# Performance work log

Measured on AMD Instinct MI355X. Metric: run time of the kernel, lower is better.

## Reference

```python
import jax, jax.numpy as jnp
import numpy as np


def setup_inputs() -> dict:
    key = jax.random.key(0)
    k1, k2 = jax.random.split(key)
    x = jax.random.normal(k1, (3000, 800, 8), dtype=jnp.float32)
    y = jax.random.normal(k2, (3000, 800, 8), dtype=jnp.float32)
    return {"x": x, "y": y}


def _cumtrapz(a):
    # torch.cumulative_trapezoid along last axis (unit spacing): len nt-1
    return jnp.cumsum(0.5 * (a[:, 1:] + a[:, :-1]), axis=1)


def _wd1d(x, y):
    nt = x.shape[0]
    # flatten (ntraces, nchannels) -> batch of independent 1D traces [N, nt]
    syn = x.reshape(nt, -1).T
    obs = y.reshape(nt, -1).T
    # per trace-pair joint minimum (torch.min(torch.min(syn), torch.min(obs)))
    mind = jnp.minimum(syn.min(axis=1, keepdims=True), obs.min(axis=1, keepdims=True))
    syn = syn - mind
    obs = obs - mind
    cdf_syn = _cumtrapz(syn)                                  # [N, nt-1]
    cdf_obs = _cumtrapz(obs)                                  # [N, nt-1]
    syn_norm = cdf_syn / jnp.sum(cdf_syn, axis=1, keepdims=True)
    obs_norm = cdf_obs / jnp.sum(cdf_obs, axis=1, keepdims=True)
    # torch.searchsorted default (right=False) == jnp side='left'
    idx = jax.vmap(lambda a, v: jnp.searchsorted(a, v, side='left'))(obs_norm, syn_norm)
    idx = jnp.minimum(idx, nt - 1)                            # clamp; t[idx] == idx since t = arange(nt)
    t_tail = jnp.arange(1, nt, dtype=jnp.int32)               # t[1:]
    diff = (t_tail[None, :] - idx).astype(syn_norm.dtype)
    return jnp.sum(diff * diff * syn_norm)


def reference(x, y):
    return _wd1d(x, y)
```

## Files before the change

kernel.cpp:

```cpp
#include <hip/hip_runtime.h>

#define NT   3000
#define NK   2999
#define NTR  6400
#define NPAIR 3200
#define CCH  64
#define KCH  47
#define GRP  8

#define TRIW 4498500.0f
#define FINF 3.4e38f

__global__ __launch_bounds__(128) void kA(
    const float* __restrict__ X, const float* __restrict__ Y,
    float* __restrict__ offx, float* __restrict__ offy,
    float* __restrict__ cmn,
    float* __restrict__ wsxA, float* __restrict__ wsyA)
{
    const int p = blockIdx.x * 128 + threadIdx.x;
    const int n = 2 * p;
    const int c = blockIdx.y;
    const int j0 = c * KCH;
    const int j1 = min(NK, j0 + KCH);

    const float2* __restrict__ X2 = (const float2*)X;
    const float2* __restrict__ Y2 = (const float2*)Y;

    float2 xp = X2[j0 * NPAIR + p];
    float2 yp = Y2[j0 * NPAIR + p];
    float mn0 = fminf(xp.x, yp.x), mn1 = fminf(xp.y, yp.y);
    float sx0 = 0.f, sx1 = 0.f, sy0 = 0.f, sy1 = 0.f;
    float wx0 = 0.f, wx1 = 0.f, wy0 = 0.f, wy1 = 0.f;

    #pragma unroll 4
    for (int j = j0; j < j1; ++j) {
        const float2 xn = X2[(j + 1) * NPAIR + p];
        const float2 yn = Y2[(j + 1) * NPAIR + p];
        const float w = (float)(NK - j);
        float s;
        s = 0.5f * (xp.x + xn.x); sx0 += s; wx0 = fmaf(s, w, wx0);
        s = 0.5f * (xp.y + xn.y); sx1 += s; wx1 = fmaf(s, w, wx1);
        s = 0.5f * (yp.x + yn.x); sy0 += s; wy0 = fmaf(s, w, wy0);
        s = 0.5f * (yp.y + yn.y); sy1 += s; wy1 = fmaf(s, w, wy1);
        mn0 = fminf(mn0, fminf(xn.x, yn.x));
        mn1 = fminf(mn1, fminf(xn.y, yn.y));
        xp = xn; yp = yn;
    }

    const int o = c * NTR + n;
    *(float2*)&offx[o] = make_float2(sx0, sx1);
    *(float2*)&offy[o] = make_float2(sy0, sy1);
    *(float2*)&cmn[o]  = make_float2(mn0, mn1);
    atomicAdd(&wsxA[n], wx0); atomicAdd(&wsxA[n + 1], wx1);
    atomicAdd(&wsyA[n], wy0); atomicAdd(&wsyA[n + 1], wy1);
}

__global__ __launch_bounds__(256) void kB(
    float* __restrict__ offx, float* __restrict__ offy,
    const float* __restrict__ cmn,
    const float* __restrict__ wsxA, const float* __restrict__ wsyA,
    float* __restrict__ mindA, float* __restrict__ SsynA,
    float* __restrict__ SobsA, float* __restrict__ out)
{
    const int n = blockIdx.x * 256 + threadIdx.x;
    if (blockIdx.x == 0 && threadIdx.x == 0) out[0] = 0.0f;

    float mn = FINF;
    for (int c = 0; c < CCH; ++c) mn = fminf(mn, cmn[c * NTR + n]);

    float rx = 0.f, ry = 0.f;
    for (int c = 0; c < CCH; ++c) {
        const int o = c * NTR + n;
        const float tx = offx[o], ty = offy[o];
        offx[o] = rx; offy[o] = ry;
        rx += tx; ry += ty;
    }

    mindA[n] = mn;
    SsynA[n] = wsxA[n] - mn * TRIW;
    SobsA[n] = wsyA[n] - mn * TRIW;
}

__global__ __launch_bounds__(256) void kC(
    const float* __restrict__ X, const float* __restrict__ Y,
    const float* __restrict__ offx, const float* __restrict__ offy,
    const float* __restrict__ mindA, const float* __restrict__ SsynA,
    const float* __restrict__ SobsA, float* __restrict__ out)
{
    const int n = blockIdx.x * 256 + threadIdx.x;
    const int c = blockIdx.y;
    const int j0 = c * KCH;
    const int j1 = min(NK, j0 + KCH);

    const float mind = mindA[n];
    const float Ssyn = SsynA[n];
    const float Sobs = SobsA[n];
    const float invS = 1.0f / Ssyn;

    float cs = offx[c * NTR + n];
    float xp = X[j0 * NTR + n];
    float acc = 0.f;

    int   mbase;
    float co;
    float ylast;
    float o[GRP];
    float co8, y8;

    #define FILL() do {                                                   \
        float yl_ = ylast, cc_ = co;                                      \
        _Pragma("unroll")                                                 \
        for (int i = 0; i < GRP; ++i) {                                   \
            const int m_ = mbase + i;                                     \
            const int ml_ = (m_ < NK) ? (m_ + 1) : NK;                    \
            const float yn_ = Y[ml_ * NTR + n];                           \
            cc_ += 0.5f * (yl_ + yn_);                                    \
            yl_ = yn_;                                                    \
            const float v_ = (cc_ - (float)(m_ + 1) * mind) * Ssyn;       \
            o[i] = (m_ < NK) ? v_ : FINF;                                 \
        }                                                                 \
        co8 = cc_; y8 = yl_;                                              \
    } while (0)

    #define COUNT(tgt, cnt) do {                                          \
        cnt = 0;                                                          \
        _Pragma("unroll")                                                 \
        for (int i = 0; i < GRP; ++i) cnt += (o[i] < (tgt)) ? 1 : 0;      \
    } while (0)

    {
        const float xn = X[(j0 + 1) * NTR + n];
        cs += 0.5f * (xp + xn); xp = xn;
        const float synp = cs - (float)(j0 + 1) * mind;
        const float target = synp * Sobs;

        int cc = 0;
        for (int c2 = min(CCH - 1, c + 2); c2 >= 1; --c2) {
            const float v = (offy[c2 * NTR + n] - (float)(c2 * KCH) * mind) * Ssyn;
            if (v < target) { cc = c2; break; }
        }
        mbase = cc * KCH;
        co = offy[cc * NTR + n];
        ylast = Y[mbase * NTR + n];
        FILL();
        int cnt; COUNT(target, cnt);
        while (cnt == GRP) {
            mbase += GRP; co = co8; ylast = y8;
            FILL();
            COUNT(target, cnt);
        }
        const float diff = (float)(j0 + 1 - (mbase + cnt));
        acc = fmaf(diff * diff, synp * invS, acc);
    }

    for (int k = j0 + 1; k < j1; ++k) {
        const float xn = X[(k + 1) * NTR + n];
        cs += 0.5f * (xp + xn); xp = xn;
        const float synp = cs - (float)(k + 1) * mind;
        const float target = synp * Sobs;

        int cnt; COUNT(target, cnt);
        while (cnt == GRP) {
            mbase += GRP; co = co8; ylast = y8;
            FILL();
            COUNT(target, cnt);
        }
        const float diff = (float)(k + 1 - (mbase + cnt));
        acc = fmaf(diff * diff, synp * invS, acc);
    }

    #undef FILL
    #undef COUNT

    __shared__ float red[256];
    red[threadIdx.x] = acc;
    __syncthreads();
    for (int s = 128; s > 0; s >>= 1) {
        if (threadIdx.x < s) red[threadIdx.x] += red[threadIdx.x + s];
        __syncthreads();
    }
    if (threadIdx.x == 0) atomicAdd(out, red[0]);
}

extern "C" void kernel_launch(void* const* d_in, const int* in_sizes, int n_in,
                              void* d_out, int out_size, void* d_ws, size_t ws_size,
                              hipStream_t stream)
{
    const float* X = (const float*)d_in[0];
    const float* Y = (const float*)d_in[1];
    float* out = (float*)d_out;

    float* w = (float*)d_ws;
    float* offx  = w;
    float* offy  = offx + CCH * NTR;
    float* cmn   = offy + CCH * NTR;
    float* wsxA  = cmn  + CCH * NTR;
    float* wsyA  = wsxA + NTR;
    float* mindA = wsyA + NTR;
    float* SsynA = mindA + NTR;
    float* SobsA = SsynA + NTR;

    hipMemsetAsync(wsxA, 0, 2 * NTR * sizeof(float), stream);

    dim3 gA(NPAIR / 128, CCH), bA(128);
    dim3 gB(NTR / 256), bB(256);
    dim3 gC(NTR / 256, CCH), bC(256);

    kA<<<gA, bA, 0, stream>>>(X, Y, offx, offy, cmn, wsxA, wsyA);
    kB<<<gB, bB, 0, stream>>>(offx, offy, cmn, wsxA, wsyA,
                              mindA, SsynA, SobsA, out);
    kC<<<gC, bC, 0, stream>>>(X, Y, offx, offy, mindA, SsynA, SobsA, out);
}
```

Before: 317.8 us.

## Precompute per-chunk search start in kB and remap kC blocks for locality

```diff
diff --git a/kernel.cpp b/kernel.cpp
--- a/kernel.cpp
+++ b/kernel.cpp
@@ -7,6 +7,7 @@
 #define CCH  64
 #define KCH  47
 #define GRP  8
+#define GT   64
 
 #define TRIW 4498500.0f
 #define FINF 3.4e38f
@@ -32,7 +33,7 @@
     float sx0 = 0.f, sx1 = 0.f, sy0 = 0.f, sy1 = 0.f;
     float wx0 = 0.f, wx1 = 0.f, wy0 = 0.f, wy1 = 0.f;
 
-    #pragma unroll 4
+    #pragma unroll 8
     for (int j = j0; j < j1; ++j) {
         const float2 xn = X2[(j + 1) * NPAIR + p];
         const float2 yn = Y2[(j + 1) * NPAIR + p];
@@ -60,35 +61,82 @@
     const float* __restrict__ cmn,
     const float* __restrict__ wsxA, const float* __restrict__ wsyA,
     float* __restrict__ mindA, float* __restrict__ SsynA,
-    float* __restrict__ SobsA, float* __restrict__ out)
-{
-    const int n = blockIdx.x * 256 + threadIdx.x;
-    if (blockIdx.x == 0 && threadIdx.x == 0) out[0] = 0.0f;
-
-    float mn = FINF;
-    for (int c = 0; c < CCH; ++c) mn = fminf(mn, cmn[c * NTR + n]);
-
-    float rx = 0.f, ry = 0.f;
-    for (int c = 0; c < CCH; ++c) {
-        const int o = c * NTR + n;
-        const float tx = offx[o], ty = offy[o];
-        offx[o] = rx; offy[o] = ry;
-        rx += tx; ry += ty;
-    }
-
-    mindA[n] = mn;
-    SsynA[n] = wsxA[n] - mn * TRIW;
-    SobsA[n] = wsyA[n] - mn * TRIW;
+    float* __restrict__ SobsA, unsigned char* __restrict__ ccA,
+    float* __restrict__ out)
+{
+    __shared__ float tA[CCH][GT + 1];
+    __shared__ float tB[CCH][GT + 1];
+    __shared__ float mindS[GT], SsS[GT], SoS[GT];
+
+    const int n0 = blockIdx.x * GT;
+    const int tid = threadIdx.x;
+    const int lane = tid & 63;
+    const int crow = tid >> 6;
+    if (blockIdx.x == 0 && tid == 0) out[0] = 0.0f;
+
+    for (int c = crow; c < CCH; c += 4)
+        tB[c][lane] = cmn[c * NTR + n0 + lane];
+    __syncthreads();
+    if (tid < GT) {
+        float mn = FINF;
+        for (int c = 0; c < CCH; ++c) mn = fminf(mn, tB[c][tid]);
+        mindS[tid] = mn;
+        mindA[n0 + tid] = mn;
+        const float ss = wsxA[n0 + tid] - mn * TRIW;
+        const float so = wsyA[n0 + tid] - mn * TRIW;
+        SsS[tid] = ss; SoS[tid] = so;
+        SsynA[n0 + tid] = ss;
+        SobsA[n0 + tid] = so;
+    }
+    __syncthreads();
+
+    for (int c = crow; c < CCH; c += 4) {
+        tA[c][lane] = offx[c * NTR + n0 + lane];
+        tB[c][lane] = offy[c * NTR + n0 + lane];
+    }
+    __syncthreads();
+    if (tid < GT) {
+        float rx = 0.f, ry = 0.f;
+        for (int c = 0; c < CCH; ++c) {
+            const float tx = tA[c][tid], ty = tB[c][tid];
+            tA[c][tid] = rx; tB[c][tid] = ry;
+            rx += tx; ry += ty;
+        }
+    }
+    __syncthreads();
+
+    for (int c = crow; c < CCH; c += 4) {
+        offx[c * NTR + n0 + lane] = tA[c][lane];
+        offy[c * NTR + n0 + lane] = tB[c][lane];
+    }
+
+    if (tid < GT) {
+        const float mind = mindS[tid], Ss = SsS[tid], So = SoS[tid];
+        int q = 0;
+        ccA[n0 + tid] = 0;
+        for (int c = 1; c < CCH; ++c) {
+            const float tgt = (tA[c][tid] - (float)(c * KCH) * mind) * So;
+            while (q + 1 < CCH) {
+                const float ov = (tB[q + 1][tid] - (float)((q + 1) * KCH) * mind) * Ss;
+                if (ov < tgt) ++q; else break;
+            }
+            ccA[c * NTR + n0 + tid] = (unsigned char)q;
+        }
+    }
 }
 
 __global__ __launch_bounds__(256) void kC(
     const float* __restrict__ X, const float* __restrict__ Y,
     const float* __restrict__ offx, const float* __restrict__ offy,
     const float* __restrict__ mindA, const float* __restrict__ SsynA,
-    const float* __restrict__ SobsA, float* __restrict__ out)
-{
-    const int n = blockIdx.x * 256 + threadIdx.x;
-    const int c = blockIdx.y;
+    const float* __restrict__ SobsA, const unsigned char* __restrict__ ccA,
+    float* __restrict__ out)
+{
+    const int bid = blockIdx.x;
+    const int g = bid & 7, r = bid >> 3;
+    const int ntile = r >> 3;
+    const int c = (g << 3) | (r & 7);
+    const int n = ntile * 256 + threadIdx.x;
     const int j0 = c * KCH;
     const int j1 = min(NK, j0 + KCH);
 
@@ -102,10 +150,16 @@
     float acc = 0.f;
 
     int   mbase;
-    float co;
-    float ylast;
+    float co, ylast;
     float o[GRP];
     float co8, y8;
+
+    {
+        const int cc = (int)ccA[c * NTR + n];
+        mbase = cc * KCH;
+        co    = offy[cc * NTR + n];
+        ylast = Y[mbase * NTR + n];
+    }
 
     #define FILL() do {                                                   \
         float yl_ = ylast, cc_ = co;                                      \
@@ -128,32 +182,9 @@
         for (int i = 0; i < GRP; ++i) cnt += (o[i] < (tgt)) ? 1 : 0;      \
     } while (0)
 
-    {
-        const float xn = X[(j0 + 1) * NTR + n];
-        cs += 0.5f * (xp + xn); xp = xn;
-        const float synp = cs - (float)(j0 + 1) * mind;
-        const float target = synp * Sobs;
-
-        int cc = 0;
-        for (int c2 = min(CCH - 1, c + 2); c2 >= 1; --c2) {
-            const float v = (offy[c2 * NTR + n] - (float)(c2 * KCH) * mind) * Ssyn;
-            if (v < target) { cc = c2; break; }
-        }
-        mbase = cc * KCH;
-        co = offy[cc * NTR + n];
-        ylast = Y[mbase * NTR + n];
-        FILL();
-        int cnt; COUNT(target, cnt);
-        while (cnt == GRP) {
-            mbase += GRP; co = co8; ylast = y8;
-            FILL();
-            COUNT(target, cnt);
-        }
-        const float diff = (float)(j0 + 1 - (mbase + cnt));
-        acc = fmaf(diff * diff, synp * invS, acc);
-    }
-
-    for (int k = j0 + 1; k < j1; ++k) {
+    FILL();
+
+    for (int k = j0; k < j1; ++k) {
         const float xn = X[(k + 1) * NTR + n];
         cs += 0.5f * (xp + xn); xp = xn;
         const float synp = cs - (float)(k + 1) * mind;
@@ -166,8 +197,9 @@
             COUNT(target, cnt);
         }
         const float diff = (float)(k + 1 - (mbase + cnt));
-        acc = fmaf(diff * diff, synp * invS, acc);
-    }
+        acc = fmaf(diff * diff, synp, acc);
+    }
+    acc *= invS;
 
     #undef FILL
     #undef COUNT
@@ -199,15 +231,16 @@
     float* mindA = wsyA + NTR;
     float* SsynA = mindA + NTR;
     float* SobsA = SsynA + NTR;
+    unsigned char* ccA = (unsigned char*)(SobsA + NTR);
 
     hipMemsetAsync(wsxA, 0, 2 * NTR * sizeof(float), stream);
 
     dim3 gA(NPAIR / 128, CCH), bA(128);
-    dim3 gB(NTR / 256), bB(256);
-    dim3 gC(NTR / 256, CCH), bC(256);
+    dim3 gB(NTR / GT), bB(256);
+    dim3 gC(1600), bC(256);
 
     kA<<<gA, bA, 0, stream>>>(X, Y, offx, offy, cmn, wsxA, wsyA);
     kB<<<gB, bB, 0, stream>>>(offx, offy, cmn, wsxA, wsyA,
-                              mindA, SsynA, SobsA, out);
-    kC<<<gC, bC, 0, stream>>>(X, Y, offx, offy, mindA, SsynA, SobsA, out);
-}
+                              mindA, SsynA, SobsA, ccA, out);
+    kC<<<gC, bC, 0, stream>>>(X, Y, offx, offy, mindA, SsynA, SobsA, ccA, out);
+}
```

Result: slower. 347.8 us (+9.5%).

## Transpose traces into row-major workspace and run wave-per-trace scan with binary search

Applied to the files above, without the earlier changes.

```diff
diff --git a/kernel.cpp b/kernel.cpp
--- a/kernel.cpp
+++ b/kernel.cpp
@@ -3,15 +3,186 @@
 #define NT   3000
 #define NK   2999
 #define NTR  6400
-#define NPAIR 3200
-#define CCH  64
-#define KCH  47
-#define GRP  8
-
 #define TRIW 4498500.0f
 #define FINF 3.4e38f
 
-__global__ __launch_bounds__(128) void kA(
+#define TSTR 3008
+#define CB   47
+
+__device__ __forceinline__ float wave_incl_scan(float v, int lane) {
+    #pragma unroll
+    for (int d = 1; d < 64; d <<= 1) {
+        float t = __shfl_up(v, d);
+        if (lane >= d) v += t;
+    }
+    return v;
+}
+__device__ __forceinline__ float wave_red_add(float v) {
+    #pragma unroll
+    for (int d = 1; d < 64; d <<= 1) v += __shfl_xor(v, d);
+    return v;
+}
+__device__ __forceinline__ float wave_red_min(float v) {
+    #pragma unroll
+    for (int d = 1; d < 64; d <<= 1) v = fminf(v, __shfl_xor(v, d));
+    return v;
+}
+
+__global__ __launch_bounds__(256) void kT(
+    const float* __restrict__ X, const float* __restrict__ Y,
+    float* __restrict__ sTx, float* __restrict__ sTy,
+    float* __restrict__ mnx, float* __restrict__ mny,
+    float* __restrict__ wsx, float* __restrict__ wsy)
+{
+    __shared__ float t[65][65];
+    const int lane = threadIdx.x & 63;
+    const int wv   = threadIdx.x >> 6;
+    const int n0 = blockIdx.x * 64;
+    const int j0 = blockIdx.y * 64;
+    const int z  = blockIdx.z;
+    const float* __restrict__ src = z ? Y : X;
+    float* __restrict__ dst = z ? sTy : sTx;
+    float* __restrict__ mnA = z ? mny : mnx;
+    float* __restrict__ wsA = z ? wsy : wsx;
+
+    #pragma unroll
+    for (int i = 0; i < 17; ++i) {
+        const int r = wv + 4 * i;
+        if (r < 65) {
+            const int jr = j0 + r;
+            if (jr < NT) t[r][lane] = src[(size_t)jr * NTR + n0 + lane];
+        }
+    }
+    __syncthreads();
+
+    const int j = j0 + lane;
+    const bool vs = (j < NK);
+    const bool va = (j < NT);
+    const float w = vs ? (float)(NK - j) : 0.f;
+
+    for (int rr = 0; rr < 16; ++rr) {
+        const int row = wv * 16 + rr;
+        const float a0 = t[lane][row];
+        const float a1 = t[lane + 1][row];
+        const float s  = vs ? 0.5f * (a0 + a1) : 0.f;
+        dst[(size_t)(n0 + row) * TSTR + j0 + lane] = s;
+        const float ws = wave_red_add(s * w);
+        const float mv = wave_red_min(va ? a0 : FINF);
+        if (lane == 0) {
+            wsA[blockIdx.y * NTR + n0 + row] = ws;
+            mnA[blockIdx.y * NTR + n0 + row] = mv;
+        }
+    }
+}
+
+__global__ __launch_bounds__(256) void kB2(
+    const float* __restrict__ mnx, const float* __restrict__ mny,
+    const float* __restrict__ wsx, const float* __restrict__ wsy,
+    float* __restrict__ mindA, float* __restrict__ SsA, float* __restrict__ SoA)
+{
+    const int n = blockIdx.x * 256 + threadIdx.x;
+    float mn = FINF, sx = 0.f, sy = 0.f;
+    for (int c = 0; c < CB; ++c) {
+        const int o = c * NTR + n;
+        mn = fminf(mn, fminf(mnx[o], mny[o]));
+        sx += wsx[o]; sy += wsy[o];
+    }
+    mindA[n] = mn;
+    SsA[n] = sx - mn * TRIW;
+    SoA[n] = sy - mn * TRIW;
+}
+
+__global__ __launch_bounds__(256) void kC2(
+    const float* __restrict__ sTx, const float* __restrict__ sTy,
+    const float* __restrict__ mindA, const float* __restrict__ SsA,
+    const float* __restrict__ SoA, float* __restrict__ partial)
+{
+    const int lane = threadIdx.x & 63;
+    const int wv   = threadIdx.x >> 6;
+    const int n = blockIdx.x * 4 + wv;
+
+    const float mind = mindA[n];
+    const float Ss = SsA[n];
+    const float So = SoA[n];
+    const float* __restrict__ sx_row = sTx + (size_t)n * TSTR;
+    const float* __restrict__ sy_row = sTy + (size_t)n * TSTR;
+
+    int   m0 = 0;
+    float co = 0.f;
+    float ov;
+
+    #define REFILL() do {                                                   \
+        const int mm = m0 + lane;                                           \
+        float v_ = (mm < NK) ? sy_row[mm] : 0.f;                            \
+        float pf_ = wave_incl_scan(v_, lane);                               \
+        ov = (mm < NK) ? (co + pf_ - (float)(mm + 1) * mind) * Ss : FINF;   \
+        co += __shfl(pf_, 63);                                              \
+    } while (0)
+
+    REFILL();
+
+    float cs = 0.f, acc = 0.f;
+    for (int b = 0; b < CB; ++b) {
+        const int j = b * 64 + lane;
+        const bool valid = (j < NK);
+        float v = valid ? sx_row[j] : 0.f;
+        float pf = wave_incl_scan(v, lane);
+        const float synp = cs + pf - (float)(j + 1) * mind;
+        cs += __shfl(pf, 63);
+        const float target = valid ? synp * So : -FINF;
+
+        bool pend = true;
+        int idx = 0;
+        while (true) {
+            const float ov_top = __shfl(ov, 63);
+            int lo = 0;
+            #pragma unroll
+            for (int s = 32; s; s >>= 1) {
+                const float pv = __shfl(ov, lo + s - 1);
+                if (pv < target) lo += s;
+            }
+            if (pend && (target <= ov_top)) { idx = m0 + lo; pend = false; }
+            if (__all(!pend)) break;
+            m0 += 64;
+            REFILL();
+        }
+        if (valid) {
+            const float diff = (float)(j + 1 - idx);
+            acc = fmaf(diff * diff, synp, acc);
+        }
+    }
+    #undef REFILL
+
+    const float tot = wave_red_add(acc);
+    __shared__ float red[4];
+    if (lane == 0) red[wv] = tot / Ss;
+    __syncthreads();
+    if (threadIdx.x == 0)
+        partial[blockIdx.x] = red[0] + red[1] + red[2] + red[3];
+}
+
+__global__ __launch_bounds__(256) void kD(
+    const float* __restrict__ partial, float* __restrict__ out)
+{
+    float v = 0.f;
+    for (int i = threadIdx.x; i < 1600; i += 256) v += partial[i];
+    __shared__ float red[256];
+    red[threadIdx.x] = v;
+    __syncthreads();
+    for (int s = 128; s > 0; s >>= 1) {
+        if (threadIdx.x < s) red[threadIdx.x] += red[threadIdx.x + s];
+        __syncthreads();
+    }
+    if (threadIdx.x == 0) out[0] = red[0];
+}
+
+#define NPAIR  3200
+#define FCH    64
+#define FKCH   47
+#define GRP    8
+#define GT     64
+
+__global__ __launch_bounds__(128) void fA(
     const float* __restrict__ X, const float* __restrict__ Y,
     float* __restrict__ offx, float* __restrict__ offy,
     float* __restrict__ cmn,
@@ -20,8 +191,8 @@
     const int p = blockIdx.x * 128 + threadIdx.x;
     const int n = 2 * p;
     const int c = blockIdx.y;
-    const int j0 = c * KCH;
-    const int j1 = min(NK, j0 + KCH);
+    const int j0 = c * FKCH;
+    const int j1 = min(NK, j0 + FKCH);
 
     const float2* __restrict__ X2 = (const float2*)X;
     const float2* __restrict__ Y2 = (const float2*)Y;
@@ -32,7 +203,7 @@
     float sx0 = 0.f, sx1 = 0.f, sy0 = 0.f, sy1 = 0.f;
     float wx0 = 0.f, wx1 = 0.f, wy0 = 0.f, wy1 = 0.f;
 
-    #pragma unroll 4
+    #pragma unroll 8
     for (int j = j0; j < j1; ++j) {
         const float2 xn = X2[(j + 1) * NPAIR + p];
         const float2 yn = Y2[(j + 1) * NPAIR + p];
@@ -55,33 +226,55 @@
     atomicAdd(&wsyA[n], wy0); atomicAdd(&wsyA[n + 1], wy1);
 }
 
-__global__ __launch_bounds__(256) void kB(
+__global__ __launch_bounds__(256) void fB(
     float* __restrict__ offx, float* __restrict__ offy,
     const float* __restrict__ cmn,
     const float* __restrict__ wsxA, const float* __restrict__ wsyA,
     float* __restrict__ mindA, float* __restrict__ SsynA,
     float* __restrict__ SobsA, float* __restrict__ out)
 {
-    const int n = blockIdx.x * 256 + threadIdx.x;
-    if (blockIdx.x == 0 && threadIdx.x == 0) out[0] = 0.0f;
-
-    float mn = FINF;
-    for (int c = 0; c < CCH; ++c) mn = fminf(mn, cmn[c * NTR + n]);
-
-    float rx = 0.f, ry = 0.f;
-    for (int c = 0; c < CCH; ++c) {
-        const int o = c * NTR + n;
-        const float tx = offx[o], ty = offy[o];
-        offx[o] = rx; offy[o] = ry;
-        rx += tx; ry += ty;
-    }
-
-    mindA[n] = mn;
-    SsynA[n] = wsxA[n] - mn * TRIW;
-    SobsA[n] = wsyA[n] - mn * TRIW;
-}
-
-__global__ __launch_bounds__(256) void kC(
+    __shared__ float tA[FCH][GT + 1];
+    __shared__ float tB[FCH][GT + 1];
+
+    const int n0 = blockIdx.x * GT;
+    const int tid = threadIdx.x;
+    const int lane = tid & 63;
+    const int crow = tid >> 6;
+    if (blockIdx.x == 0 && tid == 0) out[0] = 0.0f;
+
+    for (int c = crow; c < FCH; c += 4)
+        tB[c][lane] = cmn[c * NTR + n0 + lane];
+    __syncthreads();
+    if (tid < GT) {
+        float mn = FINF;
+        for (int c = 0; c < FCH; ++c) mn = fminf(mn, tB[c][tid]);
+        mindA[n0 + tid] = mn;
+        SsynA[n0 + tid] = wsxA[n0 + tid] - mn * TRIW;
+        SobsA[n0 + tid] = wsyA[n0 + tid] - mn * TRIW;
+    }
+    __syncthreads();
+
+    for (int c = crow; c < FCH; c += 4) {
+        tA[c][lane] = offx[c * NTR + n0 + lane];
+        tB[c][lane] = offy[c * NTR + n0 + lane];
+    }
+    __syncthreads();
+    if (tid < GT) {
+        float rx = 0.f, ry = 0.f;
+        for (int c = 0; c < FCH; ++c) {
+            const float tx = tA[c][tid], ty = tB[c][tid];
+            tA[c][tid] = rx; tB[c][tid] = ry;
+            rx += tx; ry += ty;
+        }
+    }
+    __syncthreads();
+    for (int c = crow; c < FCH; c += 4) {
+        offx[c * NTR + n0 + lane] = tA[c][lane];
+        offy[c * NTR + n0 + lane] = tB[c][lane];
+    }
+}
+
+__global__ __launch_bounds__(256) void fC(
     const float* __restrict__ X, const float* __restrict__ Y,
     const float* __restrict__ offx, const float* __restrict__ offy,
     const float* __restrict__ mindA, const float* __restrict__ SsynA,
@@ -89,8 +282,8 @@
 {
     const int n = blockIdx.x * 256 + threadIdx.x;
     const int c = blockIdx.y;
-    const int j0 = c * KCH;
-    const int j1 = min(NK, j0 + KCH);
+    const int j0 = c * FKCH;
+    const int j1 = min(NK, j0 + FKCH);
 
     const float mind = mindA[n];
     const float Ssyn = SsynA[n];
@@ -102,8 +295,7 @@
     float acc = 0.f;
 
     int   mbase;
-    float co;
-    float ylast;
+    float co, ylast;
     float o[GRP];
     float co8, y8;
 
@@ -135,11 +327,11 @@
         const float target = synp * Sobs;
 
         int cc = 0;
-        for (int c2 = min(CCH - 1, c + 2); c2 >= 1; --c2) {
-            const float v = (offy[c2 * NTR + n] - (float)(c2 * KCH) * mind) * Ssyn;
+        for (int c2 = min(FCH - 1, c + 2); c2 >= 1; --c2) {
+            const float v = (offy[c2 * NTR + n] - (float)(c2 * FKCH) * mind) * Ssyn;
             if (v < target) { cc = c2; break; }
         }
-        mbase = cc * KCH;
+        mbase = cc * FKCH;
         co = offy[cc * NTR + n];
         ylast = Y[mbase * NTR + n];
         FILL();
@@ -150,7 +342,7 @@
             COUNT(target, cnt);
         }
         const float diff = (float)(j0 + 1 - (mbase + cnt));
-        acc = fmaf(diff * diff, synp * invS, acc);
+        acc = fmaf(diff * diff, synp, acc);
     }
 
     for (int k = j0 + 1; k < j1; ++k) {
@@ -166,8 +358,9 @@
             COUNT(target, cnt);
         }
         const float diff = (float)(k + 1 - (mbase + cnt));
-        acc = fmaf(diff * diff, synp * invS, acc);
-    }
+        acc = fmaf(diff * diff, synp, acc);
+    }
+    acc *= invS;
 
     #undef FILL
     #undef COUNT
@@ -190,24 +383,45 @@
     const float* Y = (const float*)d_in[1];
     float* out = (float*)d_out;
 
-    float* w = (float*)d_ws;
-    float* offx  = w;
-    float* offy  = offx + CCH * NTR;
-    float* cmn   = offy + CCH * NTR;
-    float* wsxA  = cmn  + CCH * NTR;
-    float* wsyA  = wsxA + NTR;
-    float* mindA = wsyA + NTR;
-    float* SsynA = mindA + NTR;
-    float* SobsA = SsynA + NTR;
-
-    hipMemsetAsync(wsxA, 0, 2 * NTR * sizeof(float), stream);
-
-    dim3 gA(NPAIR / 128, CCH), bA(128);
-    dim3 gB(NTR / 256), bB(256);
-    dim3 gC(NTR / 256, CCH), bC(256);
-
-    kA<<<gA, bA, 0, stream>>>(X, Y, offx, offy, cmn, wsxA, wsyA);
-    kB<<<gB, bB, 0, stream>>>(offx, offy, cmn, wsxA, wsyA,
-                              mindA, SsynA, SobsA, out);
-    kC<<<gC, bC, 0, stream>>>(X, Y, offx, offy, mindA, SsynA, SobsA, out);
-}
+    const size_t NEW_REQ =
+        ((size_t)2 * NTR * TSTR + 4 * (size_t)CB * NTR + 3 * NTR + 1600) * 4;
+
+    if (ws_size >= NEW_REQ) {
+        float* w = (float*)d_ws;
+        float* sTx = w;
+        float* sTy = sTx + (size_t)NTR * TSTR;
+        float* mnx = sTy + (size_t)NTR * TSTR;
+        float* mny = mnx + CB * NTR;
+        float* wsx = mny + CB * NTR;
+        float* wsy = wsx + CB * NTR;
+        float* mindA = wsy + CB * NTR;
+        float* SsA = mindA + NTR;
+        float* SoA = SsA + NTR;
+        float* partial = SoA + NTR;
+
+        kT<<<dim3(100, 47, 2), 256, 0, stream>>>(X, Y, sTx, sTy, mnx, mny, wsx, wsy);
+        kB2<<<25, 256, 0, stream>>>(mnx, mny, wsx, wsy, mindA, SsA, SoA);
+        kC2<<<1600, 256, 0, stream>>>(sTx, sTy, mindA, SsA, SoA, partial);
+        kD<<<1, 256, 0, stream>>>(partial, out);
+    } else {
+        float* w = (float*)d_ws;
+        float* offx  = w;
+        float* offy  = offx + FCH * NTR;
+        float* cmn   = offy + FCH * NTR;
+        float* wsxA  = cmn  + FCH * NTR;
+        float* wsyA  = wsxA + NTR;
+        float* mindA = wsyA + NTR;
+        float* SsynA = mindA + NTR;
+        float* SobsA = SsynA + NTR;
+
+        hipMemsetAsync(wsxA, 0, 2 * NTR * sizeof(float), stream);
+
+        dim3 gA(NPAIR / 128, FCH), bA(128);
+        dim3 gB(NTR / GT), bB(256);
+        dim3 gC(NTR / 256, FCH), bC(256);
+        fA<<<gA, bA, 0, stream>>>(X, Y, offx, offy, cmn, wsxA, wsyA);
+        fB<<<gB, bB, 0, stream>>>(offx, offy, cmn, wsxA, wsyA,
+                                  mindA, SsynA, SobsA, out);
+        fC<<<gC, bC, 0, stream>>>(X, Y, offx, offy, mindA, SsynA, SobsA, out);
+    }
+}
```

Measured after the change: 358.6 us. 1.13x slower.
